# Kernel tuning notes

Hardware: AMD Instinct MI355X
Metric: run time of the kernel (lower is better)

Reference implementation:

```python
import jax, jax.numpy as jnp
import numpy as np

B, SENSORY, STATE, MOTOR = 4096, 64, 128, 32
ODE_UNFOLDS = 6
EPS = 1e-8
ELAPSED_TIME = 1.0


def setup_inputs() -> dict:
    key = jax.random.key(0)
    ks = jax.random.split(key, 20)
    u = lambda k, shape, lo, hi: jax.random.uniform(k, shape, jnp.float32, lo, hi)
    sign = lambda k, shape: jnp.where(jax.random.bernoulli(k, 0.5, shape), 1.0, -1.0).astype(jnp.float32)
    mask = lambda k, shape: (jax.random.uniform(k, shape) < 0.75).astype(jnp.float32)
    return {
        "inputs": jax.random.normal(ks[0], (B, SENSORY), jnp.float32),
        "states": jax.random.normal(ks[1], (B, STATE), jnp.float32),
        "gleak": u(ks[2], (STATE,), 0.001, 1.0),
        "vleak": u(ks[3], (STATE,), -0.2, 0.2),
        "cm": u(ks[4], (STATE,), 0.4, 0.6),
        "w": u(ks[5], (STATE, STATE), 0.001, 1.0),
        "sigma": u(ks[6], (STATE, STATE), 3.0, 8.0),
        "mu": u(ks[7], (STATE, STATE), 0.3, 0.8),
        "erev": sign(ks[8], (STATE, STATE)),
        "sensory_w": u(ks[9], (SENSORY, STATE), 0.001, 1.0),
        "sensory_sigma": u(ks[10], (SENSORY, STATE), 3.0, 8.0),
        "sensory_mu": u(ks[11], (SENSORY, STATE), 0.3, 0.8),
        "sensory_erev": sign(ks[12], (SENSORY, STATE)),
        "sparsity_mask": mask(ks[13], (STATE, STATE)),
        "sensory_sparsity_mask": mask(ks[14], (SENSORY, STATE)),
        "input_w": jnp.ones((SENSORY,), jnp.float32),
        "input_b": jnp.zeros((SENSORY,), jnp.float32),
        "output_w": jnp.ones((MOTOR,), jnp.float32),
        "output_b": jnp.zeros((MOTOR,), jnp.float32),
    }


def _syn_sigmoid(v_pre, mu, sigma):
    # v_pre: [B, P] -> [B, P, 1]; mu/sigma: [P, S]
    return jax.nn.sigmoid(sigma * (v_pre[..., None] - mu))


def reference(inputs, states, gleak, vleak, cm, w, sigma, mu, erev,
              sensory_w, sensory_sigma, sensory_mu, sensory_erev,
              sparsity_mask, sensory_sparsity_mask,
              input_w, input_b, output_w, output_b):
    # input mapping (affine); make_positive_fn = Identity (explicit constraints)
    x = inputs * input_w + input_b

    # sensory contributions (computed once, shared across unfolds)
    sens_act = sensory_w * _syn_sigmoid(x, sensory_mu, sensory_sigma)  # [B, In, S]
    sens_act = sens_act * sensory_sparsity_mask
    w_num_sensory = jnp.sum(sens_act * sensory_erev, axis=1)  # [B, S]
    w_den_sensory = jnp.sum(sens_act, axis=1)                 # [B, S]

    cm_t = cm / (ELAPSED_TIME / ODE_UNFOLDS)  # [S]

    v_pre = states
    for _ in range(ODE_UNFOLDS):
        w_act = w * _syn_sigmoid(v_pre, mu, sigma)   # [B, S, S]
        w_act = w_act * sparsity_mask
        w_numerator = jnp.sum(w_act * erev, axis=1) + w_num_sensory
        w_denominator = jnp.sum(w_act, axis=1) + w_den_sensory
        numerator = cm_t * v_pre + gleak * vleak + w_numerator
        denominator = cm_t + gleak + w_denominator
        v_pre = numerator / (denominator + EPS)

    # output mapping: slice motor neurons, then affine
    output = v_pre[:, :MOTOR] * output_w + output_b
    return output, v_pre
```

## Files before the change

### kernel.cpp

```cpp
#include <hip/hip_runtime.h>

#define LOG2E 1.4426950408889634f

constexpr int Bsz = 4096, Ssz = 128, Isz = 64, MOTOR = 32;
constexpr int BT = 8, R = 4, NT = 512;

__global__ void ltc_prep(const float* __restrict__ w, const float* __restrict__ sigma,
                         const float* __restrict__ mu, const float* __restrict__ erev,
                         const float* __restrict__ smask,
                         const float* __restrict__ sw, const float* __restrict__ ssig,
                         const float* __restrict__ smu, const float* __restrict__ serev,
                         const float* __restrict__ ssmask,
                         float4* __restrict__ A4, float4* __restrict__ B4, float4* __restrict__ W4,
                         float4* __restrict__ A4s, float4* __restrict__ B4s, float4* __restrict__ W4s)
{
  int idx = blockIdx.x * blockDim.x + threadIdx.x;
  if (idx < (Ssz / 4) * Ssz) {
    int j4 = idx >> 7, s = idx & 127;
    float4 a, b, wv;
    #pragma unroll
    for (int jj = 0; jj < 4; ++jj) {
      int e = (j4 * 4 + jj) * Ssz + s;
      float sg = sigma[e];
      (&a.x)[jj] = -sg * LOG2E;
      (&b.x)[jj] = sg * mu[e] * LOG2E;
      (&wv.x)[jj] = w[e] * smask[e] * erev[e];
    }
    A4[idx] = a; B4[idx] = b; W4[idx] = wv;
  } else if (idx < (Ssz / 4) * Ssz + (Isz / 4) * Ssz) {
    int k = idx - (Ssz / 4) * Ssz;
    int i4 = k >> 7, s = k & 127;
    float4 a, b, wv;
    #pragma unroll
    for (int jj = 0; jj < 4; ++jj) {
      int e = (i4 * 4 + jj) * Ssz + s;
      float sg = ssig[e];
      (&a.x)[jj] = -sg * LOG2E;
      (&b.x)[jj] = sg * smu[e] * LOG2E;
      (&wv.x)[jj] = sw[e] * ssmask[e] * serev[e];
    }
    A4s[k] = a; B4s[k] = b; W4s[k] = wv;
  }
}

__launch_bounds__(NT)
__global__ void ltc_main(const float* __restrict__ inputs, const float* __restrict__ states,
                         const float* __restrict__ gleak, const float* __restrict__ vleak,
                         const float* __restrict__ cmv,
                         const float* __restrict__ iw, const float* __restrict__ ib,
                         const float* __restrict__ ow, const float* __restrict__ ob,
                         const float4* __restrict__ A4, const float4* __restrict__ B4,
                         const float4* __restrict__ W4,
                         const float4* __restrict__ A4s, const float4* __restrict__ B4s,
                         const float4* __restrict__ W4s,
                         float* __restrict__ out)
{
  __shared__ float vsh[BT][Ssz];
  __shared__ float xsh[BT][Isz];
  __shared__ float redn[2][2][R][Ssz];
  __shared__ float redd[2][2][R][Ssz];

  const int t = threadIdx.x;
  const int s = t & 127;
  const int jh = (t >> 7) & 1;
  const int g = t >> 8;
  const int r0 = g * R;
  const int b0 = blockIdx.x * BT;

  for (int k = t; k < BT * Isz; k += NT) {
    int r = k >> 6, i = k & 63;
    xsh[r][i] = inputs[(b0 + r) * Isz + i] * iw[i] + ib[i];
  }
  for (int k = t; k < BT * Ssz; k += NT) {
    int r = k >> 7, ss = k & 127;
    vsh[r][ss] = states[(b0 + r) * Ssz + ss];
  }
  const float cmt = cmv[s] * 6.0f;
  const float gl = gleak[s];
  const float gv = gl * vleak[s];
  __syncthreads();

  float sn[R] = {0.f, 0.f, 0.f, 0.f}, sd[R] = {0.f, 0.f, 0.f, 0.f};
  {
    const int qb = jh * (Isz / 8);
    for (int q = 0; q < Isz / 8; ++q) {
      int iq = qb + q;
      float4 a4 = A4s[iq * Ssz + s];
      float4 b4 = B4s[iq * Ssz + s];
      float4 w4 = W4s[iq * Ssz + s];
      float xv[R][4];
      #pragma unroll
      for (int r = 0; r < R; ++r) {
        float4 xt = *(const float4*)&xsh[r0 + r][iq * 4];
        xv[r][0] = xt.x; xv[r][1] = xt.y; xv[r][2] = xt.z; xv[r][3] = xt.w;
      }
      #pragma unroll
      for (int jj = 0; jj < 4; ++jj) {
        float av = (&a4.x)[jj], bv = (&b4.x)[jj], wv = (&w4.x)[jj];
        #pragma unroll
        for (int r = 0; r < R; ++r) {
          float arg = fmaf(av, xv[r][jj], bv);
          float u = __builtin_amdgcn_exp2f(arg);
          float sig = __builtin_amdgcn_rcpf(1.0f + u);
          sn[r] = fmaf(wv, sig, sn[r]);
          sd[r] = fmaf(fabsf(wv), sig, sd[r]);
        }
      }
    }
  }

  float vnew[R];
  for (int it = 0; it < 6; ++it) {
    float num[R], den[R], vo[R];
    #pragma unroll
    for (int r = 0; r < R; ++r) { num[r] = sn[r]; den[r] = sd[r]; }
    const int qb = jh * (Ssz / 8);
    for (int q = 0; q < Ssz / 8; ++q) {
      int jq = qb + q;
      float4 a4 = A4[jq * Ssz + s];
      float4 b4 = B4[jq * Ssz + s];
      float4 w4 = W4[jq * Ssz + s];
      float vv[R][4];
      #pragma unroll
      for (int r = 0; r < R; ++r) {
        float4 vt = *(const float4*)&vsh[r0 + r][jq * 4];
        vv[r][0] = vt.x; vv[r][1] = vt.y; vv[r][2] = vt.z; vv[r][3] = vt.w;
      }
      #pragma unroll
      for (int jj = 0; jj < 4; ++jj) {
        float av = (&a4.x)[jj], bv = (&b4.x)[jj], wv = (&w4.x)[jj];
        #pragma unroll
        for (int r = 0; r < R; ++r) {
          float arg = fmaf(av, vv[r][jj], bv);
          float u = __builtin_amdgcn_exp2f(arg);
          float sig = __builtin_amdgcn_rcpf(1.0f + u);
          num[r] = fmaf(wv, sig, num[r]);
          den[r] = fmaf(fabsf(wv), sig, den[r]);
        }
      }
    }
    #pragma unroll
    for (int r = 0; r < R; ++r) {
      vo[r] = vsh[r0 + r][s];
      redn[jh][g][r][s] = num[r];
      redd[jh][g][r][s] = den[r];
    }
    __syncthreads();
    #pragma unroll
    for (int r = 0; r < R; ++r) {
      float fn = num[r] + redn[1 - jh][g][r][s];
      float fd = den[r] + redd[1 - jh][g][r][s];
      float nn = fmaf(cmt, vo[r], gv) + fn;
      float dd = cmt + gl + fd + 1e-8f;
      vnew[r] = nn * __builtin_amdgcn_rcpf(dd);
    }
    if (jh == 0) {
      #pragma unroll
      for (int r = 0; r < R; ++r) vsh[r0 + r][s] = vnew[r];
    }
    __syncthreads();
  }

  if (jh == 0) {
    #pragma unroll
    for (int r = 0; r < R; ++r) {
      int b = b0 + r0 + r;
      out[Bsz * MOTOR + b * Ssz + s] = vnew[r];
      if (s < MOTOR) out[b * MOTOR + s] = fmaf(vnew[r], ow[s], ob[s]);
    }
  }
}

extern "C" void kernel_launch(void* const* d_in, const int* in_sizes, int n_in,
                              void* d_out, int out_size, void* d_ws, size_t ws_size,
                              hipStream_t stream) {
  const float* inputs = (const float*)d_in[0];
  const float* states = (const float*)d_in[1];
  const float* gleak  = (const float*)d_in[2];
  const float* vleak  = (const float*)d_in[3];
  const float* cmv    = (const float*)d_in[4];
  const float* w      = (const float*)d_in[5];
  const float* sigma  = (const float*)d_in[6];
  const float* mu     = (const float*)d_in[7];
  const float* erev   = (const float*)d_in[8];
  const float* sw     = (const float*)d_in[9];
  const float* ssig   = (const float*)d_in[10];
  const float* smu    = (const float*)d_in[11];
  const float* serev  = (const float*)d_in[12];
  const float* smask  = (const float*)d_in[13];
  const float* ssmask = (const float*)d_in[14];
  const float* iw     = (const float*)d_in[15];
  const float* ib     = (const float*)d_in[16];
  const float* ow     = (const float*)d_in[17];
  const float* ob     = (const float*)d_in[18];

  char* ws = (char*)d_ws;
  float4* A4  = (float4*)(ws);
  float4* B4  = (float4*)(ws + 65536);
  float4* W4  = (float4*)(ws + 131072);
  float4* A4s = (float4*)(ws + 196608);
  float4* B4s = (float4*)(ws + 229376);
  float4* W4s = (float4*)(ws + 262144);
  float* out = (float*)d_out;

  constexpr int prep_items = (Ssz / 4) * Ssz + (Isz / 4) * Ssz;
  ltc_prep<<<(prep_items + 255) / 256, 256, 0, stream>>>(
      w, sigma, mu, erev, smask, sw, ssig, smu, serev, ssmask, A4, B4, W4, A4s, B4s, W4s);
  ltc_main<<<Bsz / BT, NT, 0, stream>>>(
      inputs, states, gleak, vleak, cmv, iw, ib, ow, ob, A4, B4, W4, A4s, B4s, W4s, out);
}
```

Before: 124.8 us.

## Keep recurrent synapse params in registers and split presynaptic dim four ways

Each thread now holds its 32-row slice of the recurrent A/B/W parameters in registers (96 floats) instead of re-reading them from global memory every unfold. The presynaptic dimension is split across four thread groups, with a four-way shared-memory reduction. Each block processes 16 batch rows in chunks of 4, and an extra barrier guards the state update. This removes repeated parameter loads but adds register pressure with the two-block occupancy target, plus more barriers per unfold and serialized batch chunks.

After: 115.1 us. 7.8% less time.

```diff
diff --git a/kernel.cpp b/kernel.cpp
--- a/kernel.cpp
+++ b/kernel.cpp
@@ -3,7 +3,7 @@
 #define LOG2E 1.4426950408889634f
 
 constexpr int Bsz = 4096, Ssz = 128, Isz = 64, MOTOR = 32;
-constexpr int BT = 8, R = 4, NT = 512;
+constexpr int BT = 16, R = 4, NT = 512, NQ = 4;
 
 __global__ void ltc_prep(const float* __restrict__ w, const float* __restrict__ sigma,
                          const float* __restrict__ mu, const float* __restrict__ erev,
@@ -43,7 +43,7 @@
   }
 }
 
-__launch_bounds__(NT)
+__launch_bounds__(NT, 2)
 __global__ void ltc_main(const float* __restrict__ inputs, const float* __restrict__ states,
                          const float* __restrict__ gleak, const float* __restrict__ vleak,
                          const float* __restrict__ cmv,
@@ -57,14 +57,12 @@
 {
   __shared__ float vsh[BT][Ssz];
   __shared__ float xsh[BT][Isz];
-  __shared__ float redn[2][2][R][Ssz];
-  __shared__ float redd[2][2][R][Ssz];
+  __shared__ float redn[NQ][NQ][Ssz];
+  __shared__ float redd[NQ][NQ][Ssz];
 
   const int t = threadIdx.x;
   const int s = t & 127;
-  const int jh = (t >> 7) & 1;
-  const int g = t >> 8;
-  const int r0 = g * R;
+  const int qt = t >> 7;
   const int b0 = blockIdx.x * BT;
 
   for (int k = t; k < BT * Isz; k += NT) {
@@ -78,28 +76,39 @@
   const float cmt = cmv[s] * 6.0f;
   const float gl = gleak[s];
   const float gv = gl * vleak[s];
+
+  float4 ta[8], tb[8], tw[8];
+  {
+    const float4* Ab = A4 + (qt * 8) * Ssz + s;
+    const float4* Bb = B4 + (qt * 8) * Ssz + s;
+    const float4* Wb = W4 + (qt * 8) * Ssz + s;
+    #pragma unroll
+    for (int q = 0; q < 8; ++q) {
+      ta[q] = Ab[q * Ssz];
+      tb[q] = Bb[q * Ssz];
+      tw[q] = Wb[q * Ssz];
+    }
+  }
   __syncthreads();
 
-  float sn[R] = {0.f, 0.f, 0.f, 0.f}, sd[R] = {0.f, 0.f, 0.f, 0.f};
-  {
-    const int qb = jh * (Isz / 8);
-    for (int q = 0; q < Isz / 8; ++q) {
-      int iq = qb + q;
+  #pragma unroll 1
+  for (int cb = 0; cb < BT; cb += R) {
+    float sn[R] = {0.f, 0.f, 0.f, 0.f}, sd[R] = {0.f, 0.f, 0.f, 0.f};
+    #pragma unroll
+    for (int q = 0; q < 4; ++q) {
+      int iq = qt * 4 + q;
       float4 a4 = A4s[iq * Ssz + s];
       float4 b4 = B4s[iq * Ssz + s];
       float4 w4 = W4s[iq * Ssz + s];
-      float xv[R][4];
-      #pragma unroll
-      for (int r = 0; r < R; ++r) {
-        float4 xt = *(const float4*)&xsh[r0 + r][iq * 4];
-        xv[r][0] = xt.x; xv[r][1] = xt.y; xv[r][2] = xt.z; xv[r][3] = xt.w;
-      }
+      float4 xq[R];
+      #pragma unroll
+      for (int r = 0; r < R; ++r) xq[r] = *(const float4*)&xsh[cb + r][iq * 4];
       #pragma unroll
       for (int jj = 0; jj < 4; ++jj) {
         float av = (&a4.x)[jj], bv = (&b4.x)[jj], wv = (&w4.x)[jj];
         #pragma unroll
         for (int r = 0; r < R; ++r) {
-          float arg = fmaf(av, xv[r][jj], bv);
+          float arg = fmaf(av, (&xq[r].x)[jj], bv);
           float u = __builtin_amdgcn_exp2f(arg);
           float sig = __builtin_amdgcn_rcpf(1.0f + u);
           sn[r] = fmaf(wv, sig, sn[r]);
@@ -107,67 +116,63 @@
         }
       }
     }
-  }
-
-  float vnew[R];
-  for (int it = 0; it < 6; ++it) {
-    float num[R], den[R], vo[R];
-    #pragma unroll
-    for (int r = 0; r < R; ++r) { num[r] = sn[r]; den[r] = sd[r]; }
-    const int qb = jh * (Ssz / 8);
-    for (int q = 0; q < Ssz / 8; ++q) {
-      int jq = qb + q;
-      float4 a4 = A4[jq * Ssz + s];
-      float4 b4 = B4[jq * Ssz + s];
-      float4 w4 = W4[jq * Ssz + s];
-      float vv[R][4];
-      #pragma unroll
-      for (int r = 0; r < R; ++r) {
-        float4 vt = *(const float4*)&vsh[r0 + r][jq * 4];
-        vv[r][0] = vt.x; vv[r][1] = vt.y; vv[r][2] = vt.z; vv[r][3] = vt.w;
+
+    #pragma unroll 1
+    for (int it = 0; it < 6; ++it) {
+      float num[R], den[R];
+      #pragma unroll
+      for (int r = 0; r < R; ++r) { num[r] = sn[r]; den[r] = sd[r]; }
+
+      float4 vc[R];
+      #pragma unroll
+      for (int r = 0; r < R; ++r) vc[r] = *(const float4*)&vsh[cb + r][qt * 32];
+      #pragma unroll
+      for (int q8 = 0; q8 < 8; ++q8) {
+        float4 vn_[R];
+        if (q8 < 7) {
+          #pragma unroll
+          for (int r = 0; r < R; ++r) vn_[r] = *(const float4*)&vsh[cb + r][qt * 32 + (q8 + 1) * 4];
+        }
+        #pragma unroll
+        for (int jj = 0; jj < 4; ++jj) {
+          float av = (&ta[q8].x)[jj], bv = (&tb[q8].x)[jj], wv = (&tw[q8].x)[jj];
+          #pragma unroll
+          for (int r = 0; r < R; ++r) {
+            float arg = fmaf(av, (&vc[r].x)[jj], bv);
+            float u = __builtin_amdgcn_exp2f(arg);
+            float sig = __builtin_amdgcn_rcpf(1.0f + u);
+            num[r] = fmaf(wv, sig, num[r]);
+            den[r] = fmaf(fabsf(wv), sig, den[r]);
+          }
+        }
+        if (q8 < 7) {
+          #pragma unroll
+          for (int r = 0; r < R; ++r) vc[r] = vn_[r];
+        }
       }
-      #pragma unroll
-      for (int jj = 0; jj < 4; ++jj) {
-        float av = (&a4.x)[jj], bv = (&b4.x)[jj], wv = (&w4.x)[jj];
-        #pragma unroll
-        for (int r = 0; r < R; ++r) {
-          float arg = fmaf(av, vv[r][jj], bv);
-          float u = __builtin_amdgcn_exp2f(arg);
-          float sig = __builtin_amdgcn_rcpf(1.0f + u);
-          num[r] = fmaf(wv, sig, num[r]);
-          den[r] = fmaf(fabsf(wv), sig, den[r]);
-        }
-      }
-    }
-    #pragma unroll
-    for (int r = 0; r < R; ++r) {
-      vo[r] = vsh[r0 + r][s];
-      redn[jh][g][r][s] = num[r];
-      redd[jh][g][r][s] = den[r];
-    }
-    __syncthreads();
-    #pragma unroll
-    for (int r = 0; r < R; ++r) {
-      float fn = num[r] + redn[1 - jh][g][r][s];
-      float fd = den[r] + redd[1 - jh][g][r][s];
-      float nn = fmaf(cmt, vo[r], gv) + fn;
+
+      #pragma unroll
+      for (int r = 0; r < R; ++r) { redn[qt][r][s] = num[r]; redd[qt][r][s] = den[r]; }
+      __syncthreads();
+      float fn = redn[0][qt][s] + redn[1][qt][s] + redn[2][qt][s] + redn[3][qt][s];
+      float fd = redd[0][qt][s] + redd[1][qt][s] + redd[2][qt][s] + redd[3][qt][s];
+      float vo = vsh[cb + qt][s];
+      float nn = fmaf(cmt, vo, gv) + fn;
       float dd = cmt + gl + fd + 1e-8f;
-      vnew[r] = nn * __builtin_amdgcn_rcpf(dd);
-    }
-    if (jh == 0) {
-      #pragma unroll
-      for (int r = 0; r < R; ++r) vsh[r0 + r][s] = vnew[r];
-    }
-    __syncthreads();
-  }
-
-  if (jh == 0) {
-    #pragma unroll
-    for (int r = 0; r < R; ++r) {
-      int b = b0 + r0 + r;
-      out[Bsz * MOTOR + b * Ssz + s] = vnew[r];
-      if (s < MOTOR) out[b * MOTOR + s] = fmaf(vnew[r], ow[s], ob[s]);
-    }
+      float vnew = nn * __builtin_amdgcn_rcpf(dd);
+      __syncthreads();
+      vsh[cb + qt][s] = vnew;
+      __syncthreads();
+    }
+  }
+
+  for (int k = t; k < BT * Ssz; k += NT) {
+    int r = k >> 7, ss = k & 127;
+    out[Bsz * MOTOR + (b0 + r) * Ssz + ss] = vsh[r][ss];
+  }
+  for (int k = t; k < BT * MOTOR; k += NT) {
+    int r = k >> 5, m = k & 31;
+    out[(b0 + r) * MOTOR + m] = fmaf(vsh[r][m], ow[m], ob[m]);
   }
 }
 
```
